# Performance work log

Hardware: AMD Instinct MI355X
Metric: run time of the kernel (lower is better)

The kernel has to match this reference:

```python
import jax, jax.numpy as jnp
import numpy as np

N_NODES = 100000
N_EDGES = 1600000
N_GRAPHS = 1024
DIM_IN = 128
DIM_SF = 32
DIM_OUT = 8
EPS = 1e-5


def setup_inputs() -> dict:
    key = jax.random.key(0)
    ks = jax.random.split(key, 16)
    feat = jax.random.normal(ks[0], (N_NODES, DIM_IN), dtype=jnp.float32)
    self_feat = jax.random.normal(ks[1], (N_GRAPHS, DIM_SF), dtype=jnp.float32)
    src = jax.random.randint(ks[2], (N_EDGES,), 0, N_NODES)
    dst = jax.random.randint(ks[3], (N_EDGES,), 0, N_NODES)
    node2graph = jnp.sort(jax.random.randint(ks[4], (N_NODES,), 0, N_GRAPHS))

    def lin(k, din, dout):
        s = 1.0 / np.sqrt(din)
        kw, kb = jax.random.split(k)
        W = jax.random.uniform(kw, (din, dout), minval=-s, maxval=s, dtype=jnp.float32)
        b = jax.random.uniform(kb, (dout,), minval=-s, maxval=s, dtype=jnp.float32)
        return W, b

    W1, b1 = lin(ks[5], DIM_IN, 100)
    W2, b2 = lin(ks[6], 100, 20)
    Wf1, bf1 = lin(ks[7], 20 * DIM_SF, 128)
    Wf2, bf2 = lin(ks[8], 128, 32)
    Wf3, bf3 = lin(ks[9], 32, DIM_OUT)
    g1 = jnp.ones((128,), jnp.float32); be1 = jnp.zeros((128,), jnp.float32)
    g2 = jnp.ones((32,), jnp.float32); be2 = jnp.zeros((32,), jnp.float32)
    return dict(feat=feat, self_feat=self_feat, src=src, dst=dst,
                node2graph=node2graph, W1=W1, b1=b1, W2=W2, b2=b2,
                Wf1=Wf1, bf1=bf1, g1=g1, be1=be1,
                Wf2=Wf2, bf2=bf2, g2=g2, be2=be2, Wf3=Wf3, bf3=bf3)


def _gcn_layer(h, src, dst, W, b):
    # copy_u + mean reduce: segment-mean of source features onto destinations.
    n = h.shape[0]
    msum = jax.ops.segment_sum(h[src], dst, num_segments=n)        # [N, d]
    deg = jax.ops.segment_sum(jnp.ones((src.shape[0], 1), h.dtype), dst,
                              num_segments=n)                      # [N, 1]
    # DGL: nodes with no incoming messages keep their previous 'h'.
    agg = jnp.where(deg > 0, msum / jnp.maximum(deg, 1.0), h)
    return agg @ W + b


def _bn(x, gamma, beta):
    # BatchNorm1d in training mode: biased batch statistics.
    mu = jnp.mean(x, axis=0)
    var = jnp.mean((x - mu) ** 2, axis=0)
    return (x - mu) / jnp.sqrt(var + EPS) * gamma + beta


def reference(feat, self_feat, src, dst, node2graph,
              W1, b1, W2, b2, Wf1, bf1, g1, be1, Wf2, bf2, g2, be2, Wf3, bf3):
    h = jax.nn.relu(_gcn_layer(feat, src, dst, W1, b1))            # [N, 100]
    h = jax.nn.relu(_gcn_layer(h, src, dst, W2, b2))               # [N, 20]
    # dgl.mean_nodes: per-graph mean pooling
    hsum = jax.ops.segment_sum(h, node2graph, num_segments=N_GRAPHS)
    cnt = jax.ops.segment_sum(jnp.ones((h.shape[0], 1), h.dtype), node2graph,
                              num_segments=N_GRAPHS)
    hg = hsum / jnp.maximum(cnt, 1.0)                              # [G, 20]
    # Kronecker fusion: bmm(hg[:, :, None], self_feat[:, None, :])
    fused = (hg[:, :, None] * self_feat[:, None, :]).reshape(hg.shape[0], -1)
    out = jax.nn.relu(_bn(fused @ Wf1 + bf1, g1, be1))
    out = jax.nn.relu(_bn(out @ Wf2 + bf2, g2, be2))
    return out @ Wf3 + bf3                                         # [G, 8]
```

## Files before the change

kernel.cpp:

```cpp
#include <hip/hip_runtime.h>
#include <hip/hip_fp16.h>

#define N_NODES 100000
#define N_EDGES 1600000
#define N_GRAPHS 1024
#define DIM_IN 128
#define D1 100
#define D1P 128
#define D2 20
#define D2P 32
#define DIM_SF 32
#define DF1 128
#define DF2 32
#define DOUT 8
#define EPS 1e-5f
#define NPW 8

typedef _Float16 hh2 __attribute__((ext_vector_type(2)));

__device__ __forceinline__ void fdacc(unsigned u, float& lo, float& hi) {
  const hh2 MLO = {(_Float16)1.0f, (_Float16)0.0f};
  const hh2 MHI = {(_Float16)0.0f, (_Float16)1.0f};
  hh2 h = __builtin_bit_cast(hh2, u);
  lo = __builtin_amdgcn_fdot2(h, MLO, lo, false);
  hi = __builtin_amdgcn_fdot2(h, MHI, hi, false);
}

__device__ __forceinline__ unsigned pkadd(unsigned a, unsigned b) {
  __half2 x = __builtin_bit_cast(__half2, a);
  __half2 y = __builtin_bit_cast(__half2, b);
  return __builtin_bit_cast(unsigned, __hadd2(x, y));
}

#define NBK 512
#define BW 196
#define EPB 4096
#define NBLK1 ((N_EDGES + EPB - 1) / EPB)
#define GEMM1_NB (N_NODES / 80)

__global__ void __launch_bounds__(256) k_goff(const int* __restrict__ n2g,
                                              int* __restrict__ g_off,
                                              int* __restrict__ bucket_cnt) {
  int g = blockIdx.x * 256 + threadIdx.x;
  if (g < NBK) bucket_cnt[g] = 0;
  if (g > N_GRAPHS) return;
  if (g == N_GRAPHS) { g_off[g] = N_NODES; return; }
  int lo = 0, hi = N_NODES;
  while (lo < hi) {
    int mid = (lo + hi) >> 1;
    if (n2g[mid] < g) lo = mid + 1; else hi = mid;
  }
  g_off[g] = lo;
}

__global__ void __launch_bounds__(256) k_sc_gemm(const int* __restrict__ src,
                                                 const int* __restrict__ dst,
                                                 int* __restrict__ bucket_cnt,
                                                 unsigned* __restrict__ packed_out,
                                                 const float* __restrict__ feat,
                                                 const float* __restrict__ W1,
                                                 __half* __restrict__ p1h) {
  __shared__ __align__(16) char smem[DIM_IN * D1 * 4];
  int t = threadIdx.x;
  if (blockIdx.x < NBLK1) {
    int* hist   = (int*)smem;
    int* lbase  = (int*)(smem + 2048);
    int* gbase  = (int*)(smem + 4096);
    int* ssum   = (int*)(smem + 6144);
    unsigned* sval = (unsigned*)(smem + 7168);
    int* spos   = (int*)(smem + 23552);
    int blk = blockIdx.x;
    for (int i = t; i < NBK; i += 256) hist[i] = 0;
    __syncthreads();
    int base = blk * EPB;
    unsigned pk[16]; int bn[16]; int rk[16];
#pragma unroll
    for (int r = 0; r < 16; r++) {
      int e = base + r * 256 + t;
      bn[r] = -1;
      if (e < N_EDGES) {
        int dv = dst[e];
        unsigned b = (unsigned)dv / BW;
        unsigned ld = (unsigned)dv - b * BW;
        bn[r] = (int)b;
        pk[r] = ((unsigned)src[e] << 8) | ld;
        rk[r] = atomicAdd(&hist[b], 1);
      }
    }
    __syncthreads();
    int h0 = hist[2 * t], h1 = hist[2 * t + 1];
    int s = h0 + h1;
    ssum[t] = s; __syncthreads();
    for (int off = 1; off < 256; off <<= 1) {
      int x = (t >= off) ? ssum[t - off] : 0;
      __syncthreads();
      ssum[t] += x;
      __syncthreads();
    }
    int excl = ssum[t] - s;
    lbase[2 * t] = excl;
    lbase[2 * t + 1] = excl + h0;
    gbase[2 * t]     = (h0 > 0) ? (2 * t) * EPB     + atomicAdd(&bucket_cnt[2 * t],     h0) : 0;
    gbase[2 * t + 1] = (h1 > 0) ? (2 * t + 1) * EPB + atomicAdd(&bucket_cnt[2 * t + 1], h1) : 0;
    __syncthreads();
#pragma unroll
    for (int r = 0; r < 16; r++) {
      if (bn[r] >= 0) {
        int li = lbase[bn[r]] + rk[r];
        sval[li] = pk[r];
        spos[li] = gbase[bn[r]] + rk[r];
      }
    }
    __syncthreads();
    int cnt = N_EDGES - base; if (cnt > EPB) cnt = EPB;
    for (int i = t; i < cnt; i += 256) packed_out[spos[i]] = sval[i];
  } else {
    float* w1s = (float*)smem;
    for (int i = t; i < DIM_IN * D1; i += 256) w1s[i] = W1[i];
    __syncthreads();
    if (t >= 250) return;
    int q = t % 25, ng = t / 25;
    int n0 = (int)(blockIdx.x - NBLK1) * 80 + ng * 8;
    int c0 = q * 4;
    float acc[8][4] = {{0.f}};
    const float* f0 = feat + (size_t)n0 * DIM_IN;
    for (int k = 0; k < DIM_IN; k += 4) {
      float4 w0 = *(const float4*)&w1s[(k + 0) * D1 + c0];
      float4 w1 = *(const float4*)&w1s[(k + 1) * D1 + c0];
      float4 w2 = *(const float4*)&w1s[(k + 2) * D1 + c0];
      float4 w3 = *(const float4*)&w1s[(k + 3) * D1 + c0];
#pragma unroll
      for (int j = 0; j < 8; j++) {
        float4 f = *(const float4*)(f0 + j * DIM_IN + k);
        acc[j][0] += f.x * w0.x + f.y * w1.x + f.z * w2.x + f.w * w3.x;
        acc[j][1] += f.x * w0.y + f.y * w1.y + f.z * w2.y + f.w * w3.y;
        acc[j][2] += f.x * w0.z + f.y * w1.z + f.z * w2.z + f.w * w3.z;
        acc[j][3] += f.x * w0.w + f.y * w1.w + f.z * w2.w + f.w * w3.w;
      }
    }
#pragma unroll
    for (int j = 0; j < 8; j++) {
      __half2* d2 = (__half2*)(p1h + (size_t)(n0 + j) * D1P + c0);
      d2[0] = __floats2half2_rn(acc[j][0], acc[j][1]);
      d2[1] = __floats2half2_rn(acc[j][2], acc[j][3]);
    }
  }
}

__global__ void __launch_bounds__(256) k_bfine(const unsigned* __restrict__ packed_in,
                                               const int* __restrict__ bucket_cnt,
                                               int* __restrict__ csr,
                                               int* __restrict__ deg,
                                               int* __restrict__ row_off) {
  __shared__ unsigned sval[EPB];
  __shared__ int scsr[EPB];
  __shared__ int hist[256];
  __shared__ int soff[256];
  __shared__ int cur[256];
  int b = blockIdx.x, t = threadIdx.x;
  int start = b * EPB;
  int cnt = bucket_cnt[b];
  if (cnt > EPB) cnt = EPB;
  hist[t] = 0;
  __syncthreads();
  for (int i = t; i < cnt; i += 256) {
    unsigned v = packed_in[start + i];
    sval[i] = v;
    atomicAdd(&hist[v & 255u], 1);
  }
  __syncthreads();
  int h = hist[t];
  soff[t] = h; __syncthreads();
  for (int off = 1; off < 256; off <<= 1) {
    int x = (t >= off) ? soff[t - off] : 0;
    __syncthreads();
    soff[t] += x;
    __syncthreads();
  }
  int excl = soff[t] - h;
  cur[t] = excl;
  int n = b * BW + t;
  if (t < BW && n < N_NODES) { deg[n] = h; row_off[n] = start + excl; }
  __syncthreads();
  for (int i = t; i < cnt; i += 256) {
    unsigned v = sval[i];
    int pos = atomicAdd(&cur[v & 255u], 1);
    scsr[pos] = (int)(v >> 8);
  }
  __syncthreads();
  for (int i = t; i < cnt; i += 256) csr[start + i] = scsr[i];
}

__device__ __forceinline__ void acc8d(uint4 r, float4& A, float4& B) {
  fdacc(r.x, A.x, A.y);
  fdacc(r.y, A.z, A.w);
  fdacc(r.z, B.x, B.y);
  fdacc(r.w, B.z, B.w);
}

__global__ void __launch_bounds__(256) k_agg1(const __half* __restrict__ p1h,
                                              const int* __restrict__ deg,
                                              const int* __restrict__ row_off,
                                              const int* __restrict__ csr,
                                              const float* __restrict__ b1,
                                              const float* __restrict__ W2,
                                              __half* __restrict__ p2h) {
  __shared__ float w2s[D1 * D2];
  __shared__ float b1s[D1];
  __shared__ float hbuf[4][104];
  int t = threadIdx.x;
  for (int i = t; i < D1 * D2; i += 256) w2s[i] = W2[i];
  if (t < D1) b1s[t] = b1[t];
  __syncthreads();
  int w = t >> 6, lane = t & 63;
  int g = lane >> 4, o = lane & 15;
  const size_t oh = (size_t)(o * 8);
  int p = lane / 20;
  int j20 = lane - p * 20;
  int cbeg = (p == 0) ? 0 : (p == 1) ? 33 : 66;
  int cend = (p == 0) ? 33 : (p == 1) ? 66 : 100;
  if (p >= 3) { cbeg = 0; cend = 0; }
  int n0 = (blockIdx.x * 4 + w) * NPW;
  for (int nn = 0; nn < NPW; nn++) {
    int n = n0 + nn;
    int d = deg[n], ro = row_off[n];
    float4 A = {0.f, 0.f, 0.f, 0.f}, B = {0.f, 0.f, 0.f, 0.f};
    if (d > 0) {
      for (int base = 0; base < d; base += 64) {
        int m = d - base; if (m > 64) m = 64;
        int sv = (lane < m) ? csr[ro + base + lane] : 0;
        int nr = m >> 2;
        int r = 0;
        for (; r + 3 < nr; r += 4) {
          int sA = __shfl(sv, r * 4 + g);
          int sB = __shfl(sv, r * 4 + 4 + g);
          int sC = __shfl(sv, r * 4 + 8 + g);
          int sD = __shfl(sv, r * 4 + 12 + g);
          uint4 ra = *(const uint4*)(p1h + (size_t)sA * D1P + oh);
          uint4 rb = *(const uint4*)(p1h + (size_t)sB * D1P + oh);
          uint4 rc = *(const uint4*)(p1h + (size_t)sC * D1P + oh);
          uint4 rd = *(const uint4*)(p1h + (size_t)sD * D1P + oh);
          uint4 u, v2;
          u.x = pkadd(ra.x, rb.x); u.y = pkadd(ra.y, rb.y);
          u.z = pkadd(ra.z, rb.z); u.w = pkadd(ra.w, rb.w);
          v2.x = pkadd(rc.x, rd.x); v2.y = pkadd(rc.y, rd.y);
          v2.z = pkadd(rc.z, rd.z); v2.w = pkadd(rc.w, rd.w);
          acc8d(u, A, B);
          acc8d(v2, A, B);
        }
        if (r + 1 < nr) {
          int sA = __shfl(sv, r * 4 + g);
          int sB = __shfl(sv, r * 4 + 4 + g);
          uint4 ra = *(const uint4*)(p1h + (size_t)sA * D1P + oh);
          uint4 rb = *(const uint4*)(p1h + (size_t)sB * D1P + oh);
          uint4 u;
          u.x = pkadd(ra.x, rb.x); u.y = pkadd(ra.y, rb.y);
          u.z = pkadd(ra.z, rb.z); u.w = pkadd(ra.w, rb.w);
          acc8d(u, A, B);
          r += 2;
        }
        if (r < nr) {
          int sA = __shfl(sv, r * 4 + g);
          uint4 ra = *(const uint4*)(p1h + (size_t)sA * D1P + oh);
          acc8d(ra, A, B);
        }
        int rem = m & 3;
        int sT = __shfl(sv, nr * 4 + g);
        if (rem && g < rem) {
          uint4 ra = *(const uint4*)(p1h + (size_t)sT * D1P + oh);
          acc8d(ra, A, B);
        }
      }
    } else {
      if (g == 0) {
        uint4 ra = *(const uint4*)(p1h + (size_t)n * D1P + oh);
        acc8d(ra, A, B);
      }
    }
    float v[8] = {A.x, A.y, A.z, A.w, B.x, B.y, B.z, B.w};
#pragma unroll
    for (int j = 0; j < 8; j++) {
      v[j] += __shfl_down(v[j], 32);
      v[j] += __shfl_down(v[j], 16);
    }
    if (lane < 13) {
      float inv = (d > 0) ? 1.0f / (float)d : 1.0f;
#pragma unroll
      for (int j = 0; j < 8; j++) {
        int ch = 8 * lane + j;
        if (ch < D1) hbuf[w][ch] = fmaxf(v[j] * inv + b1s[ch], 0.f);
      }
    }
    float acc = 0.f;
    for (int c = cbeg; c < cend; c++) acc += hbuf[w][c] * w2s[c * D2 + j20];
    float t1 = __shfl_down(acc, 20);
    float t2 = __shfl_down(acc, 40);
    acc += t1 + t2;
    if (lane < D2)       p2h[(size_t)n * D2P + lane] = __float2half_rn(acc);
    else if (lane < D2P) p2h[(size_t)n * D2P + lane] = __float2half_rn(0.f);
  }
}

__global__ void __launch_bounds__(512) k_agg2(const __half* __restrict__ p2h,
                                              const int* __restrict__ deg,
                                              const int* __restrict__ row_off,
                                              const int* __restrict__ csr,
                                              const float* __restrict__ b2,
                                              const int* __restrict__ g_off,
                                              float* __restrict__ hg) {
  __shared__ float ssum[D2];
  __shared__ float b2s[D2];
  int t = threadIdx.x, w = t >> 6, lane = t & 63;
  int g = blockIdx.x;
  if (t < D2) { ssum[t] = 0.f; b2s[t] = b2[t]; }
  __syncthreads();
  const unsigned* pu = (const unsigned*)p2h;
  int n_lo = g_off[g], n_hi = g_off[g + 1];
  int nn = n_hi - n_lo;
  int e16 = lane >> 2, o = lane & 3;
  bool xtra = (o == 0);
  float4 GA = {0.f, 0.f, 0.f, 0.f};
  float4 GX = {0.f, 0.f, 0.f, 0.f};
  for (int n = n_lo + w; n < n_hi; n += 8) {
    int d = deg[n], ro = row_off[n];
    float4 A = {0.f, 0.f, 0.f, 0.f};
    float4 X = {0.f, 0.f, 0.f, 0.f};
    if (d > 0) {
      for (int base = 0; base < d; base += 64) {
        int m = d - base; if (m > 64) m = 64;
        int sv = (lane < m) ? csr[ro + base + lane] : 0;
        int nr = (m + 15) >> 4;
        for (int r = 0; r < nr; r++) {
          int ei = r * 16 + e16;
          int s0 = __shfl(sv, ei);
          if (ei < m) {
            const unsigned* row = pu + (size_t)s0 * 16;
            uint2 ra = *(const uint2*)(row + 2 * o);
            fdacc(ra.x, A.x, A.y);
            fdacc(ra.y, A.z, A.w);
            if (xtra) {
              uint2 rx = *(const uint2*)(row + 8);
              fdacc(rx.x, X.x, X.y);
              fdacc(rx.y, X.z, X.w);
            }
          }
        }
      }
    } else {
      if (e16 == 0) {
        const unsigned* row = pu + (size_t)n * 16;
        uint2 ra = *(const uint2*)(row + 2 * o);
        fdacc(ra.x, A.x, A.y);
        fdacc(ra.y, A.z, A.w);
        if (xtra) {
          uint2 rx = *(const uint2*)(row + 8);
          fdacc(rx.x, X.x, X.y);
          fdacc(rx.y, X.z, X.w);
        }
      }
    }
#pragma unroll
    for (int sft = 32; sft >= 4; sft >>= 1) {
      A.x += __shfl_down(A.x, sft); A.y += __shfl_down(A.y, sft);
      A.z += __shfl_down(A.z, sft); A.w += __shfl_down(A.w, sft);
      X.x += __shfl_down(X.x, sft); X.y += __shfl_down(X.y, sft);
      X.z += __shfl_down(X.z, sft); X.w += __shfl_down(X.w, sft);
    }
    float inv = (d > 0) ? 1.0f / (float)d : 1.0f;
    if (lane < 4) {
      int ch = 4 * lane;
      GA.x += fmaxf(A.x * inv + b2s[ch + 0], 0.f);
      GA.y += fmaxf(A.y * inv + b2s[ch + 1], 0.f);
      GA.z += fmaxf(A.z * inv + b2s[ch + 2], 0.f);
      GA.w += fmaxf(A.w * inv + b2s[ch + 3], 0.f);
      if (lane == 0) {
        GX.x += fmaxf(X.x * inv + b2s[16], 0.f);
        GX.y += fmaxf(X.y * inv + b2s[17], 0.f);
        GX.z += fmaxf(X.z * inv + b2s[18], 0.f);
        GX.w += fmaxf(X.w * inv + b2s[19], 0.f);
      }
    }
  }
  if (lane < 4) {
    int ch = 4 * lane;
    atomicAdd(&ssum[ch + 0], GA.x);
    atomicAdd(&ssum[ch + 1], GA.y);
    atomicAdd(&ssum[ch + 2], GA.z);
    atomicAdd(&ssum[ch + 3], GA.w);
    if (lane == 0) {
      atomicAdd(&ssum[16], GX.x);
      atomicAdd(&ssum[17], GX.y);
      atomicAdd(&ssum[18], GX.z);
      atomicAdd(&ssum[19], GX.w);
    }
  }
  __syncthreads();
  if (t < D2) {
    float inv = (nn > 0) ? 1.0f / (float)nn : 0.f;
    hg[g * D2 + t] = ssum[t] * inv;
  }
}

__global__ void __launch_bounds__(128) k_mlp1(const float* __restrict__ hg,
                                              const float* __restrict__ sf,
                                              const float* __restrict__ Wf1,
                                              const float* __restrict__ bf1,
                                              float* __restrict__ y1) {
  __shared__ float prod[D2 * DIM_SF];
  __shared__ float hgl[D2], sfl[DIM_SF];
  int g = blockIdx.x, t = threadIdx.x;
  if (t < D2) hgl[t] = hg[g * D2 + t];
  if (t < DIM_SF) sfl[t] = sf[g * DIM_SF + t];
  __syncthreads();
  for (int i = t; i < D2 * DIM_SF; i += 128) prod[i] = hgl[i >> 5] * sfl[i & 31];
  __syncthreads();
  float acc = bf1[t];
#pragma unroll 4
  for (int k = 0; k < D2 * DIM_SF; k++) acc += prod[k] * Wf1[k * DF1 + t];
  y1[g * DF1 + t] = acc;
}

__global__ void k_bnstats(const float* __restrict__ x, int ld,
                          float* __restrict__ mu, float* __restrict__ rstd) {
  __shared__ float ssum[256], ssq[256];
  int c = blockIdx.x, t = threadIdx.x;
  float s = 0.f, q = 0.f;
  for (int r = t; r < N_GRAPHS; r += 256) { float v = x[r * ld + c]; s += v; q += v * v; }
  ssum[t] = s; ssq[t] = q; __syncthreads();
  for (int off = 128; off > 0; off >>= 1) {
    if (t < off) { ssum[t] += ssum[t + off]; ssq[t] += ssq[t + off]; }
    __syncthreads();
  }
  if (t == 0) {
    float m = ssum[0] / (float)N_GRAPHS;
    float var = ssq[0] / (float)N_GRAPHS - m * m;
    mu[c] = m;
    rstd[c] = rsqrtf(var + EPS);
  }
}

__global__ void k_mlp2(const float* __restrict__ y1, const float* __restrict__ mu1,
                       const float* __restrict__ rstd1, const float* __restrict__ g1,
                       const float* __restrict__ be1, const float* __restrict__ Wf2,
                       const float* __restrict__ bf2, float* __restrict__ y2) {
  int idx = blockIdx.x * 256 + threadIdx.x;
  int g = idx >> 5, o = idx & 31;
  float acc = bf2[o];
  for (int k = 0; k < DF1; k++) {
    float x = (y1[g * DF1 + k] - mu1[k]) * rstd1[k] * g1[k] + be1[k];
    x = fmaxf(x, 0.f);
    acc += x * Wf2[k * DF2 + o];
  }
  y2[g * DF2 + o] = acc;
}

__global__ void k_mlp3(const float* __restrict__ y2, const float* __restrict__ mu2,
                       const float* __restrict__ rstd2, const float* __restrict__ g2,
                       const float* __restrict__ be2, const float* __restrict__ Wf3,
                       const float* __restrict__ bf3, float* __restrict__ out) {
  int idx = blockIdx.x * 256 + threadIdx.x;
  int g = idx >> 3, o = idx & 7;
  float acc = bf3[o];
  for (int k = 0; k < DF2; k++) {
    float x = (y2[g * DF2 + k] - mu2[k]) * rstd2[k] * g2[k] + be2[k];
    x = fmaxf(x, 0.f);
    acc += x * Wf3[k * DOUT + o];
  }
  out[g * DOUT + o] = acc;
}

extern "C" void kernel_launch(void* const* d_in, const int* in_sizes, int n_in,
                              void* d_out, int out_size, void* d_ws, size_t ws_size,
                              hipStream_t stream) {
  const float* feat = (const float*)d_in[0];
  const float* sf   = (const float*)d_in[1];
  const int*   src  = (const int*)d_in[2];
  const int*   dst  = (const int*)d_in[3];
  const int*   n2g  = (const int*)d_in[4];
  const float* W1   = (const float*)d_in[5];
  const float* b1   = (const float*)d_in[6];
  const float* W2   = (const float*)d_in[7];
  const float* b2   = (const float*)d_in[8];
  const float* Wf1  = (const float*)d_in[9];
  const float* bf1  = (const float*)d_in[10];
  const float* g1   = (const float*)d_in[11];
  const float* be1  = (const float*)d_in[12];
  const float* Wf2  = (const float*)d_in[13];
  const float* bf2  = (const float*)d_in[14];
  const float* g2   = (const float*)d_in[15];
  const float* be2  = (const float*)d_in[16];
  const float* Wf3  = (const float*)d_in[17];
  const float* bf3  = (const float*)d_in[18];
  float* out = (float*)d_out;

  char* ws = (char*)d_ws;
  size_t off = 0;
  auto alloc = [&](size_t bytes) -> void* {
    void* p = ws + off;
    off = (off + bytes + 255) & ~(size_t)255;
    return p;
  };
  int*      bucket_cnt = (int*)alloc(NBK * 4);
  int*      g_offs   = (int*)alloc((N_GRAPHS + 1) * 4);
  float*    hg       = (float*)alloc(N_GRAPHS * D2 * 4);
  int*      deg      = (int*)alloc(N_NODES * 4);
  int*      row_off  = (int*)alloc(N_NODES * 4);
  unsigned* packed   = (unsigned*)alloc((size_t)NBK * EPB * 4);
  int*      csr      = (int*)alloc((size_t)NBK * EPB * 4);
  __half*   p1h      = (__half*)alloc((size_t)N_NODES * D1P * 2);
  __half*   p2h      = (__half*)alloc((size_t)N_NODES * D2P * 2);
  float*    y1       = (float*)alloc((size_t)N_GRAPHS * DF1 * 4);
  float*    y2       = (float*)alloc((size_t)N_GRAPHS * DF2 * 4);
  float*    mu1      = (float*)alloc(DF1 * 4);
  float*    rstd1    = (float*)alloc(DF1 * 4);
  float*    mu2      = (float*)alloc(DF2 * 4);
  float*    rstd2    = (float*)alloc(DF2 * 4);

  k_goff<<<(N_GRAPHS + 1 + 255) / 256, 256, 0, stream>>>(n2g, g_offs, bucket_cnt);
  k_sc_gemm<<<NBLK1 + GEMM1_NB, 256, 0, stream>>>(src, dst, bucket_cnt, packed,
                                                  feat, W1, p1h);
  k_bfine<<<NBK, 256, 0, stream>>>(packed, bucket_cnt, csr, deg, row_off);
  k_agg1<<<N_NODES / (4 * NPW), 256, 0, stream>>>(p1h, deg, row_off, csr, b1, W2, p2h);
  k_agg2<<<N_GRAPHS, 512, 0, stream>>>(p2h, deg, row_off, csr, b2, g_offs, hg);
  k_mlp1<<<N_GRAPHS, 128, 0, stream>>>(hg, sf, Wf1, bf1, y1);
  k_bnstats<<<DF1, 256, 0, stream>>>(y1, DF1, mu1, rstd1);
  k_mlp2<<<(N_GRAPHS * DF2) / 256, 256, 0, stream>>>(y1, mu1, rstd1, g1, be1, Wf2, bf2, y2);
  k_bnstats<<<DF2, 256, 0, stream>>>(y2, DF2, mu2, rstd2);
  k_mlp3<<<(N_GRAPHS * DOUT) / 256, 256, 0, stream>>>(y2, mu2, rstd2, g2, be2, Wf3, bf3, out);
}
```

Baseline: 403.6 us.

## Fuse batchnorm stats into MLP kernels and shrink scatter/GEMM shared memory

Removes the two separate batchnorm-statistics kernels: each MLP block now recomputes the column mean and variance of its input redundantly and folds them into a per-column scale and shift. In the scatter/GEMM kernel, the per-edge global position array in shared memory is replaced by a 16-bit bucket id, and the output slot is rebuilt from the bucket bases. The W1 tile is loaded in two halves, cutting shared memory from 51 KB to 31 KB so more blocks can be resident per CU. The trade-off is extra work: every MLP block re-reads all of y1 or y2, and the GEMM path gains an extra sync round.

After: 546.5 us. 35.4% more time.

```diff
diff --git a/kernel.cpp b/kernel.cpp
--- a/kernel.cpp
+++ b/kernel.cpp
@@ -60,7 +60,7 @@
                                                  const float* __restrict__ feat,
                                                  const float* __restrict__ W1,
                                                  __half* __restrict__ p1h) {
-  __shared__ __align__(16) char smem[DIM_IN * D1 * 4];
+  __shared__ __align__(16) char smem[31744];
   int t = threadIdx.x;
   if (blockIdx.x < NBLK1) {
     int* hist   = (int*)smem;
@@ -68,7 +68,7 @@
     int* gbase  = (int*)(smem + 4096);
     int* ssum   = (int*)(smem + 6144);
     unsigned* sval = (unsigned*)(smem + 7168);
-    int* spos   = (int*)(smem + 23552);
+    unsigned short* sbkt = (unsigned short*)(smem + 23552);
     int blk = blockIdx.x;
     for (int i = t; i < NBK; i += 256) hist[i] = 0;
     __syncthreads();
@@ -108,41 +108,52 @@
       if (bn[r] >= 0) {
         int li = lbase[bn[r]] + rk[r];
         sval[li] = pk[r];
-        spos[li] = gbase[bn[r]] + rk[r];
+        sbkt[li] = (unsigned short)bn[r];
       }
     }
     __syncthreads();
     int cnt = N_EDGES - base; if (cnt > EPB) cnt = EPB;
-    for (int i = t; i < cnt; i += 256) packed_out[spos[i]] = sval[i];
+    for (int i = t; i < cnt; i += 256) {
+      int b = sbkt[i];
+      packed_out[gbase[b] + (i - lbase[b])] = sval[i];
+    }
   } else {
     float* w1s = (float*)smem;
-    for (int i = t; i < DIM_IN * D1; i += 256) w1s[i] = W1[i];
-    __syncthreads();
-    if (t >= 250) return;
+    bool act = (t < 250);
     int q = t % 25, ng = t / 25;
     int n0 = (int)(blockIdx.x - NBLK1) * 80 + ng * 8;
     int c0 = q * 4;
     float acc[8][4] = {{0.f}};
     const float* f0 = feat + (size_t)n0 * DIM_IN;
-    for (int k = 0; k < DIM_IN; k += 4) {
-      float4 w0 = *(const float4*)&w1s[(k + 0) * D1 + c0];
-      float4 w1 = *(const float4*)&w1s[(k + 1) * D1 + c0];
-      float4 w2 = *(const float4*)&w1s[(k + 2) * D1 + c0];
-      float4 w3 = *(const float4*)&w1s[(k + 3) * D1 + c0];
+    for (int pass = 0; pass < 2; pass++) {
+      __syncthreads();
+      for (int i = t; i < 64 * D1; i += 256) w1s[i] = W1[pass * 64 * D1 + i];
+      __syncthreads();
+      if (act) {
+        int kg0 = pass * 64;
+        for (int k = 0; k < 64; k += 4) {
+          float4 w0 = *(const float4*)&w1s[(k + 0) * D1 + c0];
+          float4 w1 = *(const float4*)&w1s[(k + 1) * D1 + c0];
+          float4 w2 = *(const float4*)&w1s[(k + 2) * D1 + c0];
+          float4 w3 = *(const float4*)&w1s[(k + 3) * D1 + c0];
+#pragma unroll
+          for (int j = 0; j < 8; j++) {
+            float4 f = *(const float4*)(f0 + j * DIM_IN + kg0 + k);
+            acc[j][0] += f.x * w0.x + f.y * w1.x + f.z * w2.x + f.w * w3.x;
+            acc[j][1] += f.x * w0.y + f.y * w1.y + f.z * w2.y + f.w * w3.y;
+            acc[j][2] += f.x * w0.z + f.y * w1.z + f.z * w2.z + f.w * w3.z;
+            acc[j][3] += f.x * w0.w + f.y * w1.w + f.z * w2.w + f.w * w3.w;
+          }
+        }
+      }
+    }
+    if (act) {
 #pragma unroll
       for (int j = 0; j < 8; j++) {
-        float4 f = *(const float4*)(f0 + j * DIM_IN + k);
-        acc[j][0] += f.x * w0.x + f.y * w1.x + f.z * w2.x + f.w * w3.x;
-        acc[j][1] += f.x * w0.y + f.y * w1.y + f.z * w2.y + f.w * w3.y;
-        acc[j][2] += f.x * w0.z + f.y * w1.z + f.z * w2.z + f.w * w3.z;
-        acc[j][3] += f.x * w0.w + f.y * w1.w + f.z * w2.w + f.w * w3.w;
-      }
-    }
-#pragma unroll
-    for (int j = 0; j < 8; j++) {
-      __half2* d2 = (__half2*)(p1h + (size_t)(n0 + j) * D1P + c0);
-      d2[0] = __floats2half2_rn(acc[j][0], acc[j][1]);
-      d2[1] = __floats2half2_rn(acc[j][2], acc[j][3]);
+        __half2* d2 = (__half2*)(p1h + (size_t)(n0 + j) * D1P + c0);
+        d2[0] = __floats2half2_rn(acc[j][0], acc[j][1]);
+        d2[1] = __floats2half2_rn(acc[j][2], acc[j][3]);
+      }
     }
   }
 }
@@ -420,50 +431,80 @@
   y1[g * DF1 + t] = acc;
 }
 
-__global__ void k_bnstats(const float* __restrict__ x, int ld,
-                          float* __restrict__ mu, float* __restrict__ rstd) {
-  __shared__ float ssum[256], ssq[256];
-  int c = blockIdx.x, t = threadIdx.x;
-  float s = 0.f, q = 0.f;
-  for (int r = t; r < N_GRAPHS; r += 256) { float v = x[r * ld + c]; s += v; q += v * v; }
-  ssum[t] = s; ssq[t] = q; __syncthreads();
-  for (int off = 128; off > 0; off >>= 1) {
-    if (t < off) { ssum[t] += ssum[t + off]; ssq[t] += ssq[t + off]; }
-    __syncthreads();
-  }
-  if (t == 0) {
-    float m = ssum[0] / (float)N_GRAPHS;
-    float var = ssq[0] / (float)N_GRAPHS - m * m;
-    mu[c] = m;
-    rstd[c] = rsqrtf(var + EPS);
-  }
-}
-
-__global__ void k_mlp2(const float* __restrict__ y1, const float* __restrict__ mu1,
-                       const float* __restrict__ rstd1, const float* __restrict__ g1,
-                       const float* __restrict__ be1, const float* __restrict__ Wf2,
-                       const float* __restrict__ bf2, float* __restrict__ y2) {
-  int idx = blockIdx.x * 256 + threadIdx.x;
+__global__ void __launch_bounds__(256) k_mlp2(const float* __restrict__ y1,
+                                              const float* __restrict__ g1,
+                                              const float* __restrict__ be1,
+                                              const float* __restrict__ Wf2,
+                                              const float* __restrict__ bf2,
+                                              float* __restrict__ y2) {
+  __shared__ float nrm[DF1], sh[DF1];
+  __shared__ float ps[256], pq[256];
+  int t = threadIdx.x;
+  {
+    int c = t & 127, half = t >> 7;
+    float s = 0.f, q = 0.f;
+    for (int g = half * 512; g < half * 512 + 512; g++) {
+      float v = y1[g * DF1 + c];
+      s += v; q += v * v;
+    }
+    ps[t] = s; pq[t] = q;
+    __syncthreads();
+    if (t < DF1) {
+      float S = ps[t] + ps[t + 128];
+      float Q = pq[t] + pq[t + 128];
+      float m = S * (1.0f / N_GRAPHS);
+      float var = Q * (1.0f / N_GRAPHS) - m * m;
+      float rs = rsqrtf(var + EPS);
+      nrm[t] = g1[t] * rs;
+      sh[t] = be1[t] - m * g1[t] * rs;
+    }
+    __syncthreads();
+  }
+  int idx = blockIdx.x * 256 + t;
   int g = idx >> 5, o = idx & 31;
   float acc = bf2[o];
   for (int k = 0; k < DF1; k++) {
-    float x = (y1[g * DF1 + k] - mu1[k]) * rstd1[k] * g1[k] + be1[k];
-    x = fmaxf(x, 0.f);
+    float x = fmaxf(y1[g * DF1 + k] * nrm[k] + sh[k], 0.f);
     acc += x * Wf2[k * DF2 + o];
   }
   y2[g * DF2 + o] = acc;
 }
 
-__global__ void k_mlp3(const float* __restrict__ y2, const float* __restrict__ mu2,
-                       const float* __restrict__ rstd2, const float* __restrict__ g2,
-                       const float* __restrict__ be2, const float* __restrict__ Wf3,
-                       const float* __restrict__ bf3, float* __restrict__ out) {
-  int idx = blockIdx.x * 256 + threadIdx.x;
+__global__ void __launch_bounds__(256) k_mlp3(const float* __restrict__ y2,
+                                              const float* __restrict__ g2,
+                                              const float* __restrict__ be2,
+                                              const float* __restrict__ Wf3,
+                                              const float* __restrict__ bf3,
+                                              float* __restrict__ out) {
+  __shared__ float nrm[DF2], sh[DF2];
+  __shared__ float ps[256], pq[256];
+  int t = threadIdx.x;
+  {
+    int c = t & 31, sl = t >> 5;
+    float s = 0.f, q = 0.f;
+    for (int g = sl * 128; g < sl * 128 + 128; g++) {
+      float v = y2[g * DF2 + c];
+      s += v; q += v * v;
+    }
+    ps[t] = s; pq[t] = q;
+    __syncthreads();
+    if (t < DF2) {
+      float S = 0.f, Q = 0.f;
+#pragma unroll
+      for (int i = 0; i < 8; i++) { S += ps[t + 32 * i]; Q += pq[t + 32 * i]; }
+      float m = S * (1.0f / N_GRAPHS);
+      float var = Q * (1.0f / N_GRAPHS) - m * m;
+      float rs = rsqrtf(var + EPS);
+      nrm[t] = g2[t] * rs;
+      sh[t] = be2[t] - m * g2[t] * rs;
+    }
+    __syncthreads();
+  }
+  int idx = blockIdx.x * 256 + t;
   int g = idx >> 3, o = idx & 7;
   float acc = bf3[o];
   for (int k = 0; k < DF2; k++) {
-    float x = (y2[g * DF2 + k] - mu2[k]) * rstd2[k] * g2[k] + be2[k];
-    x = fmaxf(x, 0.f);
+    float x = fmaxf(y2[g * DF2 + k] * nrm[k] + sh[k], 0.f);
     acc += x * Wf3[k * DOUT + o];
   }
   out[g * DOUT + o] = acc;
@@ -511,10 +552,6 @@
   __half*   p2h      = (__half*)alloc((size_t)N_NODES * D2P * 2);
   float*    y1       = (float*)alloc((size_t)N_GRAPHS * DF1 * 4);
   float*    y2       = (float*)alloc((size_t)N_GRAPHS * DF2 * 4);
-  float*    mu1      = (float*)alloc(DF1 * 4);
-  float*    rstd1    = (float*)alloc(DF1 * 4);
-  float*    mu2      = (float*)alloc(DF2 * 4);
-  float*    rstd2    = (float*)alloc(DF2 * 4);
 
   k_goff<<<(N_GRAPHS + 1 + 255) / 256, 256, 0, stream>>>(n2g, g_offs, bucket_cnt);
   k_sc_gemm<<<NBLK1 + GEMM1_NB, 256, 0, stream>>>(src, dst, bucket_cnt, packed,
@@ -523,8 +560,6 @@
   k_agg1<<<N_NODES / (4 * NPW), 256, 0, stream>>>(p1h, deg, row_off, csr, b1, W2, p2h);
   k_agg2<<<N_GRAPHS, 512, 0, stream>>>(p2h, deg, row_off, csr, b2, g_offs, hg);
   k_mlp1<<<N_GRAPHS, 128, 0, stream>>>(hg, sf, Wf1, bf1, y1);
-  k_bnstats<<<DF1, 256, 0, stream>>>(y1, DF1, mu1, rstd1);
-  k_mlp2<<<(N_GRAPHS * DF2) / 256, 256, 0, stream>>>(y1, mu1, rstd1, g1, be1, Wf2, bf2, y2);
-  k_bnstats<<<DF2, 256, 0, stream>>>(y2, DF2, mu2, rstd2);
-  k_mlp3<<<(N_GRAPHS * DOUT) / 256, 256, 0, stream>>>(y2, mu2, rstd2, g2, be2, Wf3, bf3, out);
-}
+  k_mlp2<<<(N_GRAPHS * DF2) / 256, 256, 0, stream>>>(y1, g1, be1, Wf2, bf2, y2);
+  k_mlp3<<<(N_GRAPHS * DOUT) / 256, 256, 0, stream>>>(y2, g2, be2, Wf3, bf3, out);
+}
```
